# Optimization experiments

Hardware: AMD Instinct MI355X
Metric: run time of the kernel (lower is better)

Reference implementation:

```python
import jax, jax.numpy as jnp
import numpy as np

EPS = 1e-5  # torch BatchNorm2d default


def _conv(x, w, stride, pad, b=None):
    out = jax.lax.conv_general_dilated(
        x, w, (stride, stride), [(pad, pad), (pad, pad)],
        dimension_numbers=('NCHW', 'OIHW', 'NCHW'))
    if b is not None:
        out = out + b[None, :, None, None]
    return out


def _bn(x, g, b, m, v):
    # eval-mode batchnorm with running stats
    scale = g / jnp.sqrt(v + EPS)
    return (x - m[None, :, None, None]) * scale[None, :, None, None] + b[None, :, None, None]


def _silu(x):
    return x * jax.nn.sigmoid(x)


def _deform_conv3x3(x, offset, w):
    # x: [B,C,H,W]; offset: [B,18,H,W] (y,x interleaved per kernel tap, torchvision layout)
    # w: [Cout,C,3,3]; stride 1, pad 1, dilation 1, zero-padded bilinear sampling.
    B, C, H, W = x.shape
    xflat = x.reshape(B, C, H * W)
    off = offset.reshape(B, 9, 2, H, W)
    rows = jnp.arange(H, dtype=x.dtype)[:, None]   # [H,1]
    cols = jnp.arange(W, dtype=x.dtype)[None, :]   # [1,W]
    Cout = w.shape[0]
    out = jnp.zeros((B, Cout, H, W), x.dtype)
    for k in range(9):  # fixed 3x3 kernel taps
        kh, kw = k // 3, k % 3
        py = rows + (kh - 1) + off[:, k, 0]  # [B,H,W] sampling rows
        px = cols + (kw - 1) + off[:, k, 1]  # [B,H,W] sampling cols
        y0 = jnp.floor(py)
        x0 = jnp.floor(px)
        wy1 = py - y0
        wx1 = px - x0
        samp = jnp.zeros((B, C, H, W), x.dtype)
        for yi, wy in ((y0, 1.0 - wy1), (y0 + 1.0, wy1)):
            for xi, wx in ((x0, 1.0 - wx1), (x0 + 1.0, wx1)):
                valid = (yi >= 0) & (yi < H) & (xi >= 0) & (xi < W)
                idx = (jnp.clip(yi, 0, H - 1) * W + jnp.clip(xi, 0, W - 1)).astype(jnp.int32)
                v = jnp.take_along_axis(xflat, idx.reshape(B, 1, H * W), axis=2).reshape(B, C, H, W)
                samp = samp + v * (wy * wx * valid)[:, None]
        out = out + jnp.einsum('bchw,oc->bohw', samp, w[:, :, kh, kw])
    return out


def setup_inputs() -> dict:
    key = jax.random.key(0)
    ks = jax.random.split(key, 12)
    B, C1, C2, H, W = 8, 128, 256, 160, 160
    x = jax.random.normal(ks[0], (B, C1, H, W), jnp.float32)
    conv1_w = jax.random.normal(ks[1], (C2, C1, 3, 3), jnp.float32) / np.sqrt(C1 * 9)
    bn1_g = jax.random.uniform(ks[2], (C2,), jnp.float32, 0.5, 1.5)
    bn1_b = jax.random.normal(ks[3], (C2,), jnp.float32) * 0.1
    bn1_m = jax.random.normal(ks[4], (C2,), jnp.float32) * 0.1
    bn1_v = jax.random.uniform(ks[5], (C2,), jnp.float32, 0.5, 1.5)
    # small offset-conv weights so predicted offsets are O(1) pixels
    off_w = jax.random.normal(ks[6], (18, C2, 3, 3), jnp.float32) * 0.02 / np.sqrt(C2 * 9)
    off_b = jax.random.normal(ks[7], (18,), jnp.float32) * 0.1
    dconv_w = jax.random.normal(ks[8], (C2, C2, 3, 3), jnp.float32) / np.sqrt(C2 * 9)
    bn2_g = jax.random.uniform(ks[9], (C2,), jnp.float32, 0.5, 1.5)
    bn2_b = jax.random.normal(ks[10], (C2,), jnp.float32) * 0.1
    bn2_m = jax.random.normal(ks[11], (C2,), jnp.float32) * 0.1
    bn2_v = jax.random.uniform(jax.random.fold_in(key, 99), (C2,), jnp.float32, 0.5, 1.5)
    return dict(x=x, conv1_w=conv1_w, bn1_g=bn1_g, bn1_b=bn1_b, bn1_m=bn1_m, bn1_v=bn1_v,
                off_w=off_w, off_b=off_b, dconv_w=dconv_w,
                bn2_g=bn2_g, bn2_b=bn2_b, bn2_m=bn2_m, bn2_v=bn2_v)


def reference(x, conv1_w, bn1_g, bn1_b, bn1_m, bn1_v, off_w, off_b, dconv_w,
              bn2_g, bn2_b, bn2_m, bn2_v):
    h = _silu(_bn(_conv(x, conv1_w, 2, 1), bn1_g, bn1_b, bn1_m, bn1_v))   # [B,C2,80,80]
    offset = _conv(h, off_w, 1, 1, off_b)                                  # [B,18,80,80]
    y = _deform_conv3x3(h, offset, dconv_w)                                # [B,C2,80,80]
    return _silu(_bn(y, bn2_g, bn2_b, bn2_m, bn2_v))
```

## Files before the change

kernel.cpp:

```cpp
#include <hip/hip_runtime.h>
#include <hip/hip_bf16.h>


typedef __hip_bfloat16 bf16;
typedef __attribute__((ext_vector_type(8))) short short8;
typedef __attribute__((ext_vector_type(4))) float float4v;

#define EPSBN 1e-5f

__device__ __forceinline__ float bf2f(bf16 x){ return __bfloat162float(x); }
__device__ __forceinline__ float bits2f(unsigned short u){ return __uint_as_float(((unsigned)u) << 16); }
__device__ __forceinline__ float silu_(float x){ return x / (1.f + __expf(-x)); }
__device__ __forceinline__ unsigned short f2bf_bits(float f){
    union { float f; unsigned u; } uf; uf.f = f;
    unsigned r = uf.u + 0x7fff + ((uf.u >> 16) & 1);
    return (unsigned short)(r >> 16);
}

__global__ __launch_bounds__(256) void k_wdprep(const float* __restrict__ w, bf16* __restrict__ wb2)
{
    int idx = blockIdx.x * 256 + threadIdx.x;
    if (idx >= 256 * 2304) return;
    int oc  = idx / 2304;
    int r   = idx - oc * 2304;
    int tap = r >> 8;
    int c   = r & 255;
    wb2[idx] = __float2bfloat16(w[(oc * 256 + c) * 9 + tap]);
}

__global__ __launch_bounds__(256) void k_wprep1t(const float* __restrict__ w, bf16* __restrict__ wb)
{
    int idx = blockIdx.x * 256 + threadIdx.x;
    if (idx >= 256 * 1152) return;
    int oc  = idx / 1152;
    int r   = idx - oc * 1152;
    int tap = r >> 7;
    int c   = r & 127;
    wb[idx] = __float2bfloat16(w[(oc * 128 + c) * 9 + tap]);
}

__global__ __launch_bounds__(256) void k_wprep(const float* __restrict__ w, bf16* __restrict__ wb)
{
    int idx = blockIdx.x * 256 + threadIdx.x;
    if (idx >= 256 * 1152) return;
    wb[idx] = __float2bfloat16(w[idx]);
}

__global__ __launch_bounds__(256) void k_woprep2(const float* __restrict__ w, float* __restrict__ wT)
{
    int idx = blockIdx.x * 256 + threadIdx.x;
    if (idx >= 9 * 256 * 18) return;
    int oc  = idx % 18;
    int r   = idx / 18;
    int c   = r & 255;
    int tap = r >> 8;
    wT[idx] = w[(oc * 256 + c) * 9 + tap];
}

__global__ __launch_bounds__(256) void k_xprep(const float* __restrict__ x, bf16* __restrict__ xN)
{
    __shared__ short sm[64 * 132];
    const int tid  = threadIdx.x;
    const int b    = blockIdx.x / 400;
    const int pix0 = (blockIdx.x % 400) * 64;
    const int lane = tid & 63;
    const int wq   = tid >> 6;
    const float* xb = x + (size_t)b * 128 * 25600;

    #pragma unroll
    for (int i = 0; i < 32; i++){
        int c = i * 4 + wq;
        sm[lane * 132 + c] = (short)f2bf_bits(xb[c * 25600 + pix0 + lane]);
    }
    __syncthreads();

    bf16* xo = xN + ((size_t)b * 25600 + pix0) * 128;
    #pragma unroll
    for (int j = 0; j < 8; j++){
        int idx = j * 256 + tid;
        int p = idx >> 5, q = idx & 31;
        *reinterpret_cast<ushort4*>(xo + p * 128 + q * 4) =
            *reinterpret_cast<const ushort4*>(&sm[p * 132 + q * 4]);
    }
}

__global__ __launch_bounds__(256) void k_conv1n(
    const bf16* __restrict__ xN, const bf16* __restrict__ wb,
    const float* __restrict__ g, const float* __restrict__ bb,
    const float* __restrict__ mm, const float* __restrict__ vv,
    bf16* __restrict__ hN)
{
    __shared__ short A_lds[256 * 40];
    __shared__ short B_lds[64 * 40];
    __shared__ unsigned short nidx[576];
    __shared__ unsigned short nmsk[576];
    __shared__ float sc_s[256], sh_s[256];

    const int tid  = threadIdx.x;
    const int b    = blockIdx.x / 100;
    const int pix0 = (blockIdx.x % 100) * 64;
    const bf16* xb = xN + (size_t)b * 25600 * 128;

    {
        float scv = g[tid] * rsqrtf(vv[tid] + EPSBN);
        sc_s[tid] = scv;
        sh_s[tid] = bb[tid] - mm[tid] * scv;
    }

    for (int e = tid; e < 576; e += 256){
        int t = e & 63, k = e >> 6;
        int pix = pix0 + t;
        int oh = pix / 80, ow = pix % 80;
        int ih = 2 * oh + k / 3 - 1;
        int iw = 2 * ow + k % 3 - 1;
        nmsk[e] = ((ih | iw) >= 0) ? 1 : 0;
        nidx[e] = (unsigned short)(max(ih, 0) * 160 + max(iw, 0));
    }
    __syncthreads();

    const int t4   = tid >> 2;
    const int cq   = tid & 3;
    const int wv   = tid >> 6;
    const int lane = tid & 63;
    const int lrow = lane & 15;
    const int quad = lane >> 4;
    const int ocA  = tid >> 2;
    const int kqA  = tid & 3;

    uint4  pa0, pa1, pa2, pa3;
    short8 pbv;

    float4v acc[4][4];
    #pragma unroll
    for (int i = 0; i < 4; i++)
        #pragma unroll
        for (int j = 0; j < 4; j++)
            acc[i][j] = (float4v){0.f, 0.f, 0.f, 0.f};

    auto issue_pref = [&](int kc){
        const bf16* wp = wb + kc * 32 + kqA * 8;
        pa0 = *reinterpret_cast<const uint4*>(wp + (0 * 64 + ocA) * 1152);
        pa1 = *reinterpret_cast<const uint4*>(wp + (1 * 64 + ocA) * 1152);
        pa2 = *reinterpret_cast<const uint4*>(wp + (2 * 64 + ocA) * 1152);
        pa3 = *reinterpret_cast<const uint4*>(wp + (3 * 64 + ocA) * 1152);
        const int tap = kc >> 2;
        const int cb  = (kc & 3) * 32;
        const int e   = tap * 64 + t4;
        const int sp  = (int)nidx[e];
        const bool mv = nmsk[e] != 0;
        short8 v = {0, 0, 0, 0, 0, 0, 0, 0};
        if (mv) v = *reinterpret_cast<const short8*>(xb + (size_t)sp * 128 + cb + cq * 8);
        pbv = v;
    };
    auto write_stage = [&](){
        *reinterpret_cast<uint4*>(&A_lds[(0 * 64 + ocA) * 40 + kqA * 8]) = pa0;
        *reinterpret_cast<uint4*>(&A_lds[(1 * 64 + ocA) * 40 + kqA * 8]) = pa1;
        *reinterpret_cast<uint4*>(&A_lds[(2 * 64 + ocA) * 40 + kqA * 8]) = pa2;
        *reinterpret_cast<uint4*>(&A_lds[(3 * 64 + ocA) * 40 + kqA * 8]) = pa3;
        *reinterpret_cast<short8*>(&B_lds[t4 * 40 + cq * 8]) = pbv;
    };

    issue_pref(0);
    write_stage();
    __syncthreads();

    for (int kc = 0; kc < 36; kc++){
        if (kc < 35) issue_pref(kc + 1);

        short8 af[4], bfv[4];
        #pragma unroll
        for (int i = 0; i < 4; i++){
            int row = wv * 64 + i * 16 + lrow;
            af[i] = *reinterpret_cast<const short8*>(&A_lds[row * 40 + quad * 8]);
        }
        #pragma unroll
        for (int j = 0; j < 4; j++){
            bfv[j] = *reinterpret_cast<const short8*>(&B_lds[(j * 16 + lrow) * 40 + quad * 8]);
        }
        #pragma unroll
        for (int i = 0; i < 4; i++)
            #pragma unroll
            for (int j = 0; j < 4; j++)
                acc[i][j] = __builtin_amdgcn_mfma_f32_16x16x32_bf16(af[i], bfv[j], acc[i][j], 0, 0, 0);

        if (kc < 35){
            __syncthreads();
            write_stage();
            __syncthreads();
        }
    }

    #pragma unroll
    for (int i = 0; i < 4; i++){
        int oc0 = wv * 64 + i * 16 + quad * 4;
        float s0 = sc_s[oc0+0], h0 = sh_s[oc0+0];
        float s1 = sc_s[oc0+1], h1 = sh_s[oc0+1];
        float s2 = sc_s[oc0+2], h2 = sh_s[oc0+2];
        float s3 = sc_s[oc0+3], h3 = sh_s[oc0+3];
        #pragma unroll
        for (int j = 0; j < 4; j++){
            int pix = pix0 + j * 16 + lrow;
            ushort4 o;
            o.x = f2bf_bits(silu_(acc[i][j][0] * s0 + h0));
            o.y = f2bf_bits(silu_(acc[i][j][1] * s1 + h1));
            o.z = f2bf_bits(silu_(acc[i][j][2] * s2 + h2));
            o.w = f2bf_bits(silu_(acc[i][j][3] * s3 + h3));
            *reinterpret_cast<ushort4*>(hN + ((size_t)b * 6400 + pix) * 256 + oc0) = o;
        }
    }
}

__global__ __launch_bounds__(256) void k_conv1(
    const float* __restrict__ x, const bf16* __restrict__ wb,
    const float* __restrict__ g, const float* __restrict__ bb,
    const float* __restrict__ mm, const float* __restrict__ vv,
    bf16* __restrict__ hN)
{
    __shared__ short A_lds[256 * 40];
    __shared__ short B_lds[64 * 40];
    __shared__ float sc_s[256], sh_s[256];

    const int tid  = threadIdx.x;
    const int b    = blockIdx.x / 100;
    const int pix0 = (blockIdx.x % 100) * 64;
    const float* xb = x + b * (128 * 25600);

    {
        float scv = g[tid] * rsqrtf(vv[tid] + EPSBN);
        sc_s[tid] = scv;
        sh_s[tid] = bb[tid] - mm[tid] * scv;
    }

    const int k_in = tid & 31;
    const int prow = tid >> 5;
    int oh8[8], ow8[8];
    #pragma unroll
    for (int p = 0; p < 8; p++){
        int pix = pix0 + prow + p * 8;
        oh8[p] = pix / 80; ow8[p] = pix % 80;
    }

    const int wv   = tid >> 6;
    const int lane = tid & 63;
    const int lrow = lane & 15;
    const int quad = lane >> 4;

    float4v acc[4][4];
    #pragma unroll
    for (int i = 0; i < 4; i++)
        #pragma unroll
        for (int j = 0; j < 4; j++)
            acc[i][j] = (float4v){0.f, 0.f, 0.f, 0.f};

    for (int kc = 0; kc < 36; kc++){
        const int k0 = kc * 32;
        __syncthreads();

        #pragma unroll
        for (int p2 = 0; p2 < 4; p2++){
            int idx = p2 * 256 + tid;
            int oc  = idx >> 2;
            int kq  = idx & 3;
            *reinterpret_cast<uint4*>(&A_lds[oc * 40 + kq * 8]) =
                *reinterpret_cast<const uint4*>(wb + oc * 1152 + k0 + kq * 8);
        }

        {
            int kk  = k0 + k_in;
            int c   = kk / 9;
            int tap = kk - 9 * c;
            int kh  = tap / 3 - 1;
            int kw  = tap - 3 * (tap / 3) - 1;
            const float* xc = xb + c * 25600;
            #pragma unroll
            for (int p = 0; p < 8; p++){
                int ih = 2 * oh8[p] + kh;
                int iw = 2 * ow8[p] + kw;
                float v = 0.f;
                if ((ih | iw) >= 0) v = xc[ih * 160 + iw];
                B_lds[(prow + p * 8) * 40 + k_in] = (short)f2bf_bits(v);
            }
        }
        __syncthreads();

        short8 af[4], bfv[4];
        #pragma unroll
        for (int i = 0; i < 4; i++){
            int row = wv * 64 + i * 16 + lrow;
            af[i] = *reinterpret_cast<const short8*>(&A_lds[row * 40 + quad * 8]);
        }
        #pragma unroll
        for (int j = 0; j < 4; j++){
            bfv[j] = *reinterpret_cast<const short8*>(&B_lds[(j * 16 + lrow) * 40 + quad * 8]);
        }
        #pragma unroll
        for (int i = 0; i < 4; i++)
            #pragma unroll
            for (int j = 0; j < 4; j++)
                acc[i][j] = __builtin_amdgcn_mfma_f32_16x16x32_bf16(af[i], bfv[j], acc[i][j], 0, 0, 0);
    }

    #pragma unroll
    for (int i = 0; i < 4; i++){
        int oc0 = wv * 64 + i * 16 + quad * 4;
        float s0 = sc_s[oc0+0], h0 = sh_s[oc0+0];
        float s1 = sc_s[oc0+1], h1 = sh_s[oc0+1];
        float s2 = sc_s[oc0+2], h2 = sh_s[oc0+2];
        float s3 = sc_s[oc0+3], h3 = sh_s[oc0+3];
        #pragma unroll
        for (int j = 0; j < 4; j++){
            int pix = pix0 + j * 16 + lrow;
            ushort4 o;
            o.x = f2bf_bits(silu_(acc[i][j][0] * s0 + h0));
            o.y = f2bf_bits(silu_(acc[i][j][1] * s1 + h1));
            o.z = f2bf_bits(silu_(acc[i][j][2] * s2 + h2));
            o.w = f2bf_bits(silu_(acc[i][j][3] * s3 + h3));
            *reinterpret_cast<ushort4*>(hN + (b * 6400 + pix) * 256 + oc0) = o;
        }
    }
}

__global__ __launch_bounds__(256) void k_off_v(
    const bf16* __restrict__ hN, const float* __restrict__ wT,
    const float* __restrict__ bias, float* __restrict__ off)
{
    __shared__ float red[4 * 18 * 64];

    const int tid   = threadIdx.x;
    const int b     = blockIdx.x & 7;
    const int pix0  = (blockIdx.x >> 3) * 64;
    const int lane  = tid & 63;
    const int wv    = tid >> 6;
    const int cbase = __builtin_amdgcn_readfirstlane(wv << 6);

    const int pix = pix0 + lane;
    const int oh  = pix / 80, ow = pix % 80;

    float acc[18];
    #pragma unroll
    for (int o = 0; o < 18; o++) acc[o] = 0.f;

    for (int tap = 0; tap < 9; tap++){
        int ih = oh + tap / 3 - 1, iw = ow + tap % 3 - 1;
        bool val = ((unsigned)ih < 80u) && ((unsigned)iw < 80u);
        int  sp  = min(max(ih, 0), 79) * 80 + min(max(iw, 0), 79);
        float m  = val ? 1.f : 0.f;
        const bf16*  hp = hN + (size_t)(b * 6400 + sp) * 256 + cbase;
        const float* wp = wT + (tap * 256 + cbase) * 18;
        for (int cs = 0; cs < 64; cs += 4){
            ushort4 hv = *reinterpret_cast<const ushort4*>(hp + cs);
            float h0 = bits2f(hv.x) * m, h1 = bits2f(hv.y) * m,
                  h2 = bits2f(hv.z) * m, h3 = bits2f(hv.w) * m;
            const float* w0 = wp + cs * 18;
            #pragma unroll
            for (int o = 0; o < 18; o++){
                acc[o] += h0 * w0[o] + h1 * w0[18 + o] + h2 * w0[36 + o] + h3 * w0[54 + o];
            }
        }
    }

    #pragma unroll
    for (int o = 0; o < 18; o++)
        red[(wv * 18 + o) * 64 + lane] = acc[o];
    __syncthreads();

    for (int i = tid; i < 18 * 64; i += 256){
        int o = i >> 6, p = i & 63;
        float s = red[(0 * 18 + o) * 64 + p] + red[(1 * 18 + o) * 64 + p]
                + red[(2 * 18 + o) * 64 + p] + red[(3 * 18 + o) * 64 + p] + bias[o];
        off[(b * 18 + o) * 6400 + pix0 + p] = s;
    }
}

__global__ __launch_bounds__(256) void k_dconv_nhwc(
    const bf16* __restrict__ hN, const float* __restrict__ off,
    const bf16* __restrict__ wb2,
    const float* __restrict__ g, const float* __restrict__ bb,
    const float* __restrict__ mm, const float* __restrict__ vv,
    float* __restrict__ out)
{
    __shared__ short   A_lds[256 * 40];
    __shared__ short   B_lds[64 * 40];
    __shared__ ushort4 sidxu[576];
    __shared__ ushort4 swtu [576];
    __shared__ float   sc_s[256], sh_s[256];

    const int tid  = threadIdx.x;
    const int b    = blockIdx.x & 7;
    const int pix0 = (blockIdx.x >> 3) * 64;
    const bf16* hb = hN + b * (6400 * 256);

    {
        float scv = g[tid] * rsqrtf(vv[tid] + EPSBN);
        sc_s[tid] = scv;
        sh_s[tid] = bb[tid] - mm[tid] * scv;
    }

    for (int e = tid; e < 576; e += 256){
        int t = e & 63, k = e >> 6;
        int pix = pix0 + t;
        int oh = pix / 80, ow = pix % 80;
        int kh = k / 3, kw = k % 3;
        float oy = off[(b * 18 + 2 * k    ) * 6400 + pix];
        float ox = off[(b * 18 + 2 * k + 1) * 6400 + pix];
        float py = (float)(oh + kh - 1) + oy;
        float px = (float)(ow + kw - 1) + ox;
        float y0f = floorf(py), x0f = floorf(px);
        float wy1 = py - y0f,  wx1 = px - x0f;
        int y0 = (int)y0f, x0 = (int)x0f;
        unsigned short ii[4], ww[4];
        #pragma unroll
        for (int cy = 0; cy < 2; cy++){
            int   yy = y0 + cy;
            float wy = cy ? wy1 : 1.f - wy1;
            bool  vy = (yy >= 0) && (yy < 80);
            int   yc = min(max(yy, 0), 79);
            #pragma unroll
            for (int cx = 0; cx < 2; cx++){
                int   xx = x0 + cx;
                float wx = cx ? wx1 : 1.f - wx1;
                bool  vx = (xx >= 0) && (xx < 80);
                int   xc = min(max(xx, 0), 79);
                int ci = cy * 2 + cx;
                ii[ci] = (unsigned short)(yc * 80 + xc);
                ww[ci] = f2bf_bits((vy && vx) ? wy * wx : 0.f);
            }
        }
        ushort4 iv; iv.x = ii[0]; iv.y = ii[1]; iv.z = ii[2]; iv.w = ii[3];
        ushort4 wv_; wv_.x = ww[0]; wv_.y = ww[1]; wv_.z = ww[2]; wv_.w = ww[3];
        sidxu[e] = iv;
        swtu [e] = wv_;
    }
    __syncthreads();

    const int t4   = tid >> 2;
    const int cq   = tid & 3;
    const int wv   = tid >> 6;
    const int lane = tid & 63;
    const int lrow = lane & 15;
    const int quad = lane >> 4;
    const int ocA  = tid >> 2;
    const int kqA  = tid & 3;

    const bf16* wA = wb2 + (size_t)ocA * 2304 + kqA * 8;

    float w0, w1, w2, w3;
    const bf16 *p0, *p1, *p2, *p3;
    auto load_tap_state = [&](int tap){
        const int e = tap * 64 + t4;
        ushort4 ipk = sidxu[e];
        ushort4 wpk = swtu[e];
        w0 = bits2f(wpk.x); w1 = bits2f(wpk.y);
        w2 = bits2f(wpk.z); w3 = bits2f(wpk.w);
        p0 = hb + (int)ipk.x * 256 + cq * 8;
        p1 = hb + (int)ipk.y * 256 + cq * 8;
        p2 = hb + (int)ipk.z * 256 + cq * 8;
        p3 = hb + (int)ipk.w * 256 + cq * 8;
    };

    uint4  pa0, pa1, pa2, pa3;
    short8 pb0, pb1, pb2, pb3;

    auto issue_pref = [&](int kc){
        const bf16* wp = wA + kc * 32;
        pa0 = *reinterpret_cast<const uint4*>(wp);
        pa1 = *reinterpret_cast<const uint4*>(wp + (size_t)64 * 2304);
        pa2 = *reinterpret_cast<const uint4*>(wp + (size_t)128 * 2304);
        pa3 = *reinterpret_cast<const uint4*>(wp + (size_t)192 * 2304);
        const int co = (kc & 7) * 32;
        pb0 = *reinterpret_cast<const short8*>(p0 + co);
        pb1 = *reinterpret_cast<const short8*>(p1 + co);
        pb2 = *reinterpret_cast<const short8*>(p2 + co);
        pb3 = *reinterpret_cast<const short8*>(p3 + co);
    };

    float4v acc[4][4];
    #pragma unroll
    for (int i = 0; i < 4; i++)
        #pragma unroll
        for (int j = 0; j < 4; j++)
            acc[i][j] = (float4v){0.f, 0.f, 0.f, 0.f};

    load_tap_state(0);
    issue_pref(0);

    for (int tap = 0; tap < 9; tap++){
        for (int sub = 0; sub < 8; sub++){
            const int kc = tap * 8 + sub;

            short8 ob;
            #pragma unroll
            for (int el = 0; el < 8; el++){
                float f = w0 * bits2f((unsigned short)pb0[el])
                        + w1 * bits2f((unsigned short)pb1[el])
                        + w2 * bits2f((unsigned short)pb2[el])
                        + w3 * bits2f((unsigned short)pb3[el]);
                ob[el] = (short)f2bf_bits(f);
            }

            __syncthreads();

            *reinterpret_cast<uint4*>(&A_lds[(0 * 64 + ocA) * 40 + kqA * 8]) = pa0;
            *reinterpret_cast<uint4*>(&A_lds[(1 * 64 + ocA) * 40 + kqA * 8]) = pa1;
            *reinterpret_cast<uint4*>(&A_lds[(2 * 64 + ocA) * 40 + kqA * 8]) = pa2;
            *reinterpret_cast<uint4*>(&A_lds[(3 * 64 + ocA) * 40 + kqA * 8]) = pa3;
            *reinterpret_cast<short8*>(&B_lds[t4 * 40 + cq * 8]) = ob;

            __syncthreads();

            if (kc < 71){
                if (sub == 7) load_tap_state(tap + 1);
                issue_pref(kc + 1);
            }

            short8 af[4], bfv[4];
            #pragma unroll
            for (int i = 0; i < 4; i++){
                int row = wv * 64 + i * 16 + lrow;
                af[i] = *reinterpret_cast<const short8*>(&A_lds[row * 40 + quad * 8]);
            }
            #pragma unroll
            for (int j = 0; j < 4; j++){
                bfv[j] = *reinterpret_cast<const short8*>(&B_lds[(j * 16 + lrow) * 40 + quad * 8]);
            }
            #pragma unroll
            for (int i = 0; i < 4; i++)
                #pragma unroll
                for (int j = 0; j < 4; j++)
                    acc[i][j] = __builtin_amdgcn_mfma_f32_16x16x32_bf16(af[i], bfv[j], acc[i][j], 0, 0, 0);
        }
    }

    #pragma unroll
    for (int i = 0; i < 4; i++){
        #pragma unroll
        for (int r = 0; r < 4; r++){
            int oc = wv * 64 + i * 16 + quad * 4 + r;
            float scv = sc_s[oc], shv = sh_s[oc];
            #pragma unroll
            for (int j = 0; j < 4; j++){
                int pix = pix0 + j * 16 + lrow;
                out[(b * 256 + oc) * 6400 + pix] = silu_(acc[i][j][r] * scv + shv);
            }
        }
    }
}

extern "C" void kernel_launch(void* const* d_in, const int* in_sizes, int n_in,
                              void* d_out, int out_size, void* d_ws, size_t ws_size,
                              hipStream_t stream)
{
    (void)in_sizes; (void)n_in; (void)out_size;

    const float* x  = (const float*)d_in[0];
    const float* w1 = (const float*)d_in[1];
    const float* g1 = (const float*)d_in[2];
    const float* b1 = (const float*)d_in[3];
    const float* m1 = (const float*)d_in[4];
    const float* v1 = (const float*)d_in[5];
    const float* wo = (const float*)d_in[6];
    const float* bo = (const float*)d_in[7];
    const float* wd = (const float*)d_in[8];
    const float* g2 = (const float*)d_in[9];
    const float* b2 = (const float*)d_in[10];
    const float* m2 = (const float*)d_in[11];
    const float* v2 = (const float*)d_in[12];
    float* outp = (float*)d_out;

    char*  wsb  = (char*)d_ws;
    bf16*  hNb  = (bf16*) wsb;
    float* obuf = (float*)(wsb + 26214400);
    bf16*  wb2b = (bf16*) (wsb + 29900800);
    bf16*  wbb  = (bf16*) (wsb + 31080448);
    float* wTof = (float*)(wsb + 31670272);
    bf16*  xNb  = (bf16*) (wsb + 31836160);

    const size_t need_primary = 84264960;

    hipLaunchKernelGGL(k_wdprep,  dim3(2304), dim3(256), 0, stream, wd, wb2b);
    hipLaunchKernelGGL(k_woprep2, dim3(162),  dim3(256), 0, stream, wo, wTof);

    if (ws_size >= need_primary){
        hipLaunchKernelGGL(k_wprep1t, dim3(1152), dim3(256), 0, stream, w1, wbb);
        hipLaunchKernelGGL(k_xprep,   dim3(3200), dim3(256), 0, stream, x, xNb);
        hipLaunchKernelGGL(k_conv1n,  dim3(800),  dim3(256), 0, stream, xNb, wbb, g1, b1, m1, v1, hNb);
    } else {
        hipLaunchKernelGGL(k_wprep,   dim3(1152), dim3(256), 0, stream, w1, wbb);
        hipLaunchKernelGGL(k_conv1,   dim3(800),  dim3(256), 0, stream, x, wbb, g1, b1, m1, v1, hNb);
    }

    hipLaunchKernelGGL(k_off_v,     dim3(800), dim3(256), 0, stream, hNb, wTof, bo, obuf);
    hipLaunchKernelGGL(k_dconv_nhwc,dim3(800), dim3(256), 0, stream, hNb, obuf, wb2b, g2, b2, m2, v2, outp);
}
```

Measured before the change: 551.9 us.

## Fuse offset conv into deformable conv kernel and interleave conv1 block order

The offset-prediction 3x3 conv is computed inside the deformable conv kernel for each 64-pixel tile, with its partial sums reduced through LDS reused from the GEMM staging buffers. This removes a separate kernel launch and the global round trip of the offset tensor. The conv1 kernel's block-to-(batch, pixel) mapping is also changed to interleave batches across consecutive blocks. In exchange, the offset conv now sits serially at the start of each dconv block and adds register pressure, which can lower occupancy for the main GEMM.

After: 581.8 us. +5.4%, slower.

```diff
diff --git a/kernel.cpp b/kernel.cpp
--- a/kernel.cpp
+++ b/kernel.cpp
@@ -97,8 +97,8 @@
     __shared__ float sc_s[256], sh_s[256];
 
     const int tid  = threadIdx.x;
-    const int b    = blockIdx.x / 100;
-    const int pix0 = (blockIdx.x % 100) * 64;
+    const int b    = blockIdx.x & 7;
+    const int pix0 = (blockIdx.x >> 3) * 64;
     const bf16* xb = xN + (size_t)b * 25600 * 128;
 
     {
@@ -320,61 +320,9 @@
     }
 }
 
-__global__ __launch_bounds__(256) void k_off_v(
+__global__ __launch_bounds__(256) void k_dconv_nhwc(
     const bf16* __restrict__ hN, const float* __restrict__ wT,
-    const float* __restrict__ bias, float* __restrict__ off)
-{
-    __shared__ float red[4 * 18 * 64];
-
-    const int tid   = threadIdx.x;
-    const int b     = blockIdx.x & 7;
-    const int pix0  = (blockIdx.x >> 3) * 64;
-    const int lane  = tid & 63;
-    const int wv    = tid >> 6;
-    const int cbase = __builtin_amdgcn_readfirstlane(wv << 6);
-
-    const int pix = pix0 + lane;
-    const int oh  = pix / 80, ow = pix % 80;
-
-    float acc[18];
-    #pragma unroll
-    for (int o = 0; o < 18; o++) acc[o] = 0.f;
-
-    for (int tap = 0; tap < 9; tap++){
-        int ih = oh + tap / 3 - 1, iw = ow + tap % 3 - 1;
-        bool val = ((unsigned)ih < 80u) && ((unsigned)iw < 80u);
-        int  sp  = min(max(ih, 0), 79) * 80 + min(max(iw, 0), 79);
-        float m  = val ? 1.f : 0.f;
-        const bf16*  hp = hN + (size_t)(b * 6400 + sp) * 256 + cbase;
-        const float* wp = wT + (tap * 256 + cbase) * 18;
-        for (int cs = 0; cs < 64; cs += 4){
-            ushort4 hv = *reinterpret_cast<const ushort4*>(hp + cs);
-            float h0 = bits2f(hv.x) * m, h1 = bits2f(hv.y) * m,
-                  h2 = bits2f(hv.z) * m, h3 = bits2f(hv.w) * m;
-            const float* w0 = wp + cs * 18;
-            #pragma unroll
-            for (int o = 0; o < 18; o++){
-                acc[o] += h0 * w0[o] + h1 * w0[18 + o] + h2 * w0[36 + o] + h3 * w0[54 + o];
-            }
-        }
-    }
-
-    #pragma unroll
-    for (int o = 0; o < 18; o++)
-        red[(wv * 18 + o) * 64 + lane] = acc[o];
-    __syncthreads();
-
-    for (int i = tid; i < 18 * 64; i += 256){
-        int o = i >> 6, p = i & 63;
-        float s = red[(0 * 18 + o) * 64 + p] + red[(1 * 18 + o) * 64 + p]
-                + red[(2 * 18 + o) * 64 + p] + red[(3 * 18 + o) * 64 + p] + bias[o];
-        off[(b * 18 + o) * 6400 + pix0 + p] = s;
-    }
-}
-
-__global__ __launch_bounds__(256) void k_dconv_nhwc(
-    const bf16* __restrict__ hN, const float* __restrict__ off,
-    const bf16* __restrict__ wb2,
+    const float* __restrict__ obias, const bf16* __restrict__ wb2,
     const float* __restrict__ g, const float* __restrict__ bb,
     const float* __restrict__ mm, const float* __restrict__ vv,
     float* __restrict__ out)
@@ -390,19 +338,64 @@
     const int pix0 = (blockIdx.x >> 3) * 64;
     const bf16* hb = hN + b * (6400 * 256);
 
+    float* red  = reinterpret_cast<float*>(A_lds);
+    float* offs = reinterpret_cast<float*>(B_lds);
+
     {
         float scv = g[tid] * rsqrtf(vv[tid] + EPSBN);
         sc_s[tid] = scv;
         sh_s[tid] = bb[tid] - mm[tid] * scv;
     }
+
+    {
+        const int lane  = tid & 63;
+        const int wvv   = tid >> 6;
+        const int cbase = __builtin_amdgcn_readfirstlane(wvv << 6);
+        const int pix = pix0 + lane;
+        const int oh  = pix / 80, ow = pix % 80;
+
+        float oacc[18];
+        #pragma unroll
+        for (int o = 0; o < 18; o++) oacc[o] = 0.f;
+
+        for (int tap = 0; tap < 9; tap++){
+            int ih = oh + tap / 3 - 1, iw = ow + tap % 3 - 1;
+            bool val = ((unsigned)ih < 80u) && ((unsigned)iw < 80u);
+            int  sp  = min(max(ih, 0), 79) * 80 + min(max(iw, 0), 79);
+            float m  = val ? 1.f : 0.f;
+            const bf16*  hp = hb + (size_t)sp * 256 + cbase;
+            const float* wp = wT + (tap * 256 + cbase) * 18;
+            for (int cs = 0; cs < 64; cs += 4){
+                ushort4 hv = *reinterpret_cast<const ushort4*>(hp + cs);
+                float h0 = bits2f(hv.x) * m, h1 = bits2f(hv.y) * m,
+                      h2 = bits2f(hv.z) * m, h3 = bits2f(hv.w) * m;
+                const float* w0 = wp + cs * 18;
+                #pragma unroll
+                for (int o = 0; o < 18; o++){
+                    oacc[o] += h0 * w0[o] + h1 * w0[18 + o] + h2 * w0[36 + o] + h3 * w0[54 + o];
+                }
+            }
+        }
+        #pragma unroll
+        for (int o = 0; o < 18; o++)
+            red[(wvv * 18 + o) * 64 + lane] = oacc[o];
+    }
+    __syncthreads();
+
+    for (int i = tid; i < 18 * 64; i += 256){
+        int o = i >> 6, p = i & 63;
+        offs[i] = red[(0 * 18 + o) * 64 + p] + red[(1 * 18 + o) * 64 + p]
+                + red[(2 * 18 + o) * 64 + p] + red[(3 * 18 + o) * 64 + p] + obias[o];
+    }
+    __syncthreads();
 
     for (int e = tid; e < 576; e += 256){
         int t = e & 63, k = e >> 6;
         int pix = pix0 + t;
         int oh = pix / 80, ow = pix % 80;
         int kh = k / 3, kw = k % 3;
-        float oy = off[(b * 18 + 2 * k    ) * 6400 + pix];
-        float ox = off[(b * 18 + 2 * k + 1) * 6400 + pix];
+        float oy = offs[(2 * k    ) * 64 + t];
+        float ox = offs[(2 * k + 1) * 64 + t];
         float py = (float)(oh + kh - 1) + oy;
         float px = (float)(ow + kw - 1) + ox;
         float y0f = floorf(py), x0f = floorf(px);
@@ -569,7 +562,6 @@
 
     char*  wsb  = (char*)d_ws;
     bf16*  hNb  = (bf16*) wsb;
-    float* obuf = (float*)(wsb + 26214400);
     bf16*  wb2b = (bf16*) (wsb + 29900800);
     bf16*  wbb  = (bf16*) (wsb + 31080448);
     float* wTof = (float*)(wsb + 31670272);
@@ -589,6 +581,6 @@
         hipLaunchKernelGGL(k_conv1,   dim3(800),  dim3(256), 0, stream, x, wbb, g1, b1, m1, v1, hNb);
     }
 
-    hipLaunchKernelGGL(k_off_v,     dim3(800), dim3(256), 0, stream, hNb, wTof, bo, obuf);
-    hipLaunchKernelGGL(k_dconv_nhwc,dim3(800), dim3(256), 0, stream, hNb, obuf, wb2b, g2, b2, m2, v2, outp);
-}
+    hipLaunchKernelGGL(k_dconv_nhwc, dim3(800), dim3(256), 0, stream,
+                       hNb, wTof, bo, wb2b, g2, b2, m2, v2, outp);
+}
```

## Compute offset conv with bf16 MFMA and interleave conv1 blocks across batch

Applied to the files above, without the earlier changes.

The 18-channel offset convolution moves from scalar FP32 FMAs with an LDS cross-wave reduction to 16x16x32 bf16 MFMA instructions. The offset weights are pre-packed into MFMA fragment layout and padded to 32 output channels. Each wave now handles 16 pixels over the full 2304-long reduction, so the shared-memory reduction and barrier go away. Separately, conv1 block indexing is changed to interleave batches (b = blockIdx & 7), which likely changes cache locality. Rounding the offset weights to bf16 reduces offset precision, and padding wastes close to half of the MFMA work.

Result: faster. 474.9 us (-13.9%).

```diff
diff --git a/kernel.cpp b/kernel.cpp
--- a/kernel.cpp
+++ b/kernel.cpp
@@ -46,15 +46,21 @@
     wb[idx] = __float2bfloat16(w[idx]);
 }
 
-__global__ __launch_bounds__(256) void k_woprep2(const float* __restrict__ w, float* __restrict__ wT)
+__global__ __launch_bounds__(256) void k_woprepm(const float* __restrict__ w, bf16* __restrict__ wm)
 {
     int idx = blockIdx.x * 256 + threadIdx.x;
-    if (idx >= 9 * 256 * 18) return;
-    int oc  = idx % 18;
-    int r   = idx / 18;
-    int c   = r & 255;
-    int tap = r >> 8;
-    wT[idx] = w[(oc * 256 + c) * 9 + tap];
+    if (idx >= 2 * 72 * 512) return;
+    int j    = idx & 7;
+    int lane = (idx >> 3) & 63;
+    int frag = idx >> 9;
+    int half = frag / 72;
+    int kc   = frag - half * 72;
+    int oc   = half * 16 + (lane & 15);
+    int kk   = kc * 32 + (lane >> 4) * 8 + j;
+    int tap  = kk >> 8;
+    int c    = kk & 255;
+    float v  = (oc < 18) ? w[(oc * 256 + c) * 9 + tap] : 0.f;
+    wm[idx] = __float2bfloat16(v);
 }
 
 __global__ __launch_bounds__(256) void k_xprep(const float* __restrict__ x, bf16* __restrict__ xN)
@@ -97,8 +103,8 @@
     __shared__ float sc_s[256], sh_s[256];
 
     const int tid  = threadIdx.x;
-    const int b    = blockIdx.x / 100;
-    const int pix0 = (blockIdx.x % 100) * 64;
+    const int b    = blockIdx.x & 7;
+    const int pix0 = (blockIdx.x >> 3) * 64;
     const bf16* xb = xN + (size_t)b * 25600 * 128;
 
     {
@@ -320,55 +326,53 @@
     }
 }
 
-__global__ __launch_bounds__(256) void k_off_v(
-    const bf16* __restrict__ hN, const float* __restrict__ wT,
+__global__ __launch_bounds__(256) void k_off_m(
+    const bf16* __restrict__ hN, const bf16* __restrict__ wm,
     const float* __restrict__ bias, float* __restrict__ off)
 {
-    __shared__ float red[4 * 18 * 64];
-
-    const int tid   = threadIdx.x;
-    const int b     = blockIdx.x & 7;
-    const int pix0  = (blockIdx.x >> 3) * 64;
-    const int lane  = tid & 63;
-    const int wv    = tid >> 6;
-    const int cbase = __builtin_amdgcn_readfirstlane(wv << 6);
-
-    const int pix = pix0 + lane;
+    const int tid  = threadIdx.x;
+    const int b    = blockIdx.x & 7;
+    const int pix0 = (blockIdx.x >> 3) * 64 + (tid >> 6) * 16;
+    const int lane = tid & 63;
+    const int l15  = lane & 15;
+    const int ksl  = lane >> 4;
+    const bf16* hb = hN + b * (6400 * 256);
+
+    const int pix = pix0 + l15;
     const int oh  = pix / 80, ow = pix % 80;
 
-    float acc[18];
-    #pragma unroll
-    for (int o = 0; o < 18; o++) acc[o] = 0.f;
+    float4v acc0 = {0.f, 0.f, 0.f, 0.f};
+    float4v acc1 = {0.f, 0.f, 0.f, 0.f};
 
     for (int tap = 0; tap < 9; tap++){
-        int ih = oh + tap / 3 - 1, iw = ow + tap % 3 - 1;
-        bool val = ((unsigned)ih < 80u) && ((unsigned)iw < 80u);
-        int  sp  = min(max(ih, 0), 79) * 80 + min(max(iw, 0), 79);
-        float m  = val ? 1.f : 0.f;
-        const bf16*  hp = hN + (size_t)(b * 6400 + sp) * 256 + cbase;
-        const float* wp = wT + (tap * 256 + cbase) * 18;
-        for (int cs = 0; cs < 64; cs += 4){
-            ushort4 hv = *reinterpret_cast<const ushort4*>(hp + cs);
-            float h0 = bits2f(hv.x) * m, h1 = bits2f(hv.y) * m,
-                  h2 = bits2f(hv.z) * m, h3 = bits2f(hv.w) * m;
-            const float* w0 = wp + cs * 18;
-            #pragma unroll
-            for (int o = 0; o < 18; o++){
-                acc[o] += h0 * w0[o] + h1 * w0[18 + o] + h2 * w0[36 + o] + h3 * w0[54 + o];
-            }
-        }
-    }
-
-    #pragma unroll
-    for (int o = 0; o < 18; o++)
-        red[(wv * 18 + o) * 64 + lane] = acc[o];
-    __syncthreads();
-
-    for (int i = tid; i < 18 * 64; i += 256){
-        int o = i >> 6, p = i & 63;
-        float s = red[(0 * 18 + o) * 64 + p] + red[(1 * 18 + o) * 64 + p]
-                + red[(2 * 18 + o) * 64 + p] + red[(3 * 18 + o) * 64 + p] + bias[o];
-        off[(b * 18 + o) * 6400 + pix0 + p] = s;
+        const int ih = oh + tap / 3 - 1;
+        const int iw = ow + tap % 3 - 1;
+        const bool val = ((unsigned)ih < 80u) && ((unsigned)iw < 80u);
+        const int sp  = val ? (ih * 80 + iw) : 0;
+        const bf16* hp = hb + (size_t)sp * 256 + ksl * 8;
+        const bf16* wp = wm + (size_t)tap * 8 * 512 + lane * 8;
+        #pragma unroll
+        for (int sub = 0; sub < 8; sub++){
+            short8 bf_ = {0, 0, 0, 0, 0, 0, 0, 0};
+            if (val) bf_ = *reinterpret_cast<const short8*>(hp + sub * 32);
+            short8 a0 = *reinterpret_cast<const short8*>(wp + sub * 512);
+            short8 a1 = *reinterpret_cast<const short8*>(wp + 72 * 512 + sub * 512);
+            acc0 = __builtin_amdgcn_mfma_f32_16x16x32_bf16(a0, bf_, acc0, 0, 0, 0);
+            acc1 = __builtin_amdgcn_mfma_f32_16x16x32_bf16(a1, bf_, acc1, 0, 0, 0);
+        }
+    }
+
+    #pragma unroll
+    for (int r = 0; r < 4; r++){
+        int oc = ksl * 4 + r;
+        off[((size_t)b * 18 + oc) * 6400 + pix] = acc0[r] + bias[oc];
+    }
+    if (ksl == 0){
+        #pragma unroll
+        for (int r = 0; r < 2; r++){
+            int oc = 16 + r;
+            off[((size_t)b * 18 + oc) * 6400 + pix] = acc1[r] + bias[oc];
+        }
     }
 }
 
@@ -572,13 +576,13 @@
     float* obuf = (float*)(wsb + 26214400);
     bf16*  wb2b = (bf16*) (wsb + 29900800);
     bf16*  wbb  = (bf16*) (wsb + 31080448);
-    float* wTof = (float*)(wsb + 31670272);
+    bf16*  wmof = (bf16*) (wsb + 31670272);
     bf16*  xNb  = (bf16*) (wsb + 31836160);
 
     const size_t need_primary = 84264960;
 
     hipLaunchKernelGGL(k_wdprep,  dim3(2304), dim3(256), 0, stream, wd, wb2b);
-    hipLaunchKernelGGL(k_woprep2, dim3(162),  dim3(256), 0, stream, wo, wTof);
+    hipLaunchKernelGGL(k_woprepm, dim3(288),  dim3(256), 0, stream, wo, wmof);
 
     if (ws_size >= need_primary){
         hipLaunchKernelGGL(k_wprep1t, dim3(1152), dim3(256), 0, stream, w1, wbb);
@@ -589,6 +593,6 @@
         hipLaunchKernelGGL(k_conv1,   dim3(800),  dim3(256), 0, stream, x, wbb, g1, b1, m1, v1, hNb);
     }
 
-    hipLaunchKernelGGL(k_off_v,     dim3(800), dim3(256), 0, stream, hNb, wTof, bo, obuf);
+    hipLaunchKernelGGL(k_off_m,     dim3(800), dim3(256), 0, stream, hNb, wmof, bo, obuf);
     hipLaunchKernelGGL(k_dconv_nhwc,dim3(800), dim3(256), 0, stream, hNb, obuf, wb2b, g2, b2, m2, v2, outp);
 }
```
